# Optimization experiments

Measured on AMD Instinct MI355X. Metric: run time of the kernel, lower is better.

Reference implementation:

```python
import jax, jax.numpy as jnp
import numpy as np

N_HEADS = 16
ROPE_BASE = 10000.0


def _rope_tables(T, head_dim, dtype):
    inv_freq = 1.0 / (ROPE_BASE ** (jnp.arange(0, head_dim, 2, dtype=jnp.float32) / head_dim))
    t = jnp.arange(T, dtype=jnp.float32)
    freqs = jnp.outer(t, inv_freq)              # (T, head_dim/2)
    emb = jnp.concatenate([freqs, freqs], -1)   # (T, head_dim)
    return jnp.cos(emb).astype(dtype), jnp.sin(emb).astype(dtype)


def _rotate_half(x):
    x1, x2 = jnp.split(x, 2, axis=-1)
    return jnp.concatenate([-x2, x1], axis=-1)


def setup_inputs() -> dict:
    key = jax.random.key(0)
    k1, k2, k3 = jax.random.split(key, 3)
    B, T, C = 2, 2048, 2048
    x = jax.random.normal(k1, (B, T, C), dtype=jnp.float32)
    Wqkv = jax.random.normal(k2, (C, 3 * C), dtype=jnp.float32) * (1.0 / np.sqrt(C))
    Wproj = jax.random.normal(k3, (C, C), dtype=jnp.float32) * (1.0 / np.sqrt(C))
    return {"x": x, "Wqkv": Wqkv, "Wproj": Wproj}


def reference(x, Wqkv, Wproj):
    B, T, C = x.shape
    H = N_HEADS
    D = C // H
    qkv = jnp.einsum('btc,cd->btd', x, Wqkv)            # (B,T,3C)
    q, k, v = jnp.split(qkv, 3, axis=-1)
    # (B,T,C) -> (B,H,T,D)
    q = q.reshape(B, T, H, D).transpose(0, 2, 1, 3)
    k = k.reshape(B, T, H, D).transpose(0, 2, 1, 3)
    v = v.reshape(B, T, H, D).transpose(0, 2, 1, 3)
    cos, sin = _rope_tables(T, D, x.dtype)              # (T,D) each
    q = q * cos + _rotate_half(q) * sin
    k = k * cos + _rotate_half(k) * sin
    scale = 1.0 / jnp.sqrt(jnp.asarray(D, x.dtype))
    att = jnp.einsum('bhqd,bhkd->bhqk', q, k) * scale   # (B,H,T,T)
    causal = jnp.tril(jnp.ones((T, T), dtype=bool))
    att = jnp.where(causal, att, jnp.asarray(-jnp.inf, att.dtype))
    att = jax.nn.softmax(att, axis=-1)
    y = jnp.einsum('bhqk,bhkd->bhqd', att, v)           # (B,H,T,D)
    y = y.transpose(0, 2, 1, 3).reshape(B, T, C)
    return jnp.einsum('btc,cd->btd', y, Wproj)
```

## Files before the change

kernel.cpp:

```cpp
#include <hip/hip_runtime.h>
#include <stdint.h>

#define T_SEQ 2048
#define NH 16
#define HD 128
#define CC 2048
#define N3 6144
#define MM 4096

typedef short bf16x8 __attribute__((ext_vector_type(8)));
typedef float f32x4 __attribute__((ext_vector_type(4)));
typedef float f32x16 __attribute__((ext_vector_type(16)));
typedef unsigned int u32x4 __attribute__((ext_vector_type(4)));

__device__ __forceinline__ unsigned short f2bf(float f) {
  unsigned int u = __float_as_uint(f);
  u += 0x7FFF + ((u >> 16) & 1);
  return (unsigned short)(u >> 16);
}
__device__ __forceinline__ float bf2f(unsigned short h) {
  return __uint_as_float(((unsigned int)h) << 16);
}
__device__ __forceinline__ unsigned int cvt_pk_bf16(float lo, float hi) {
  unsigned int r;
  asm("v_cvt_pk_bf16_f32 %0, %1, %2" : "=v"(r) : "v"(lo), "v"(hi));
  return r;
}

__global__ __launch_bounds__(256) void k_prep(const float* __restrict__ Wqkv,
                                              unsigned short* __restrict__ WqkvT,
                                              const float* __restrict__ Wproj,
                                              unsigned short* __restrict__ WprojT,
                                              const float* __restrict__ x,
                                              unsigned short* __restrict__ xb) {
  __shared__ float tile[32][33];
  const int bi = blockIdx.x;
  const int tx = threadIdx.x & 31, ty = threadIdx.x >> 5;
  if (bi < 16384) {
    const float* in;
    unsigned short* out;
    int k0, n0, N;
    if (bi < 12288) {
      in = Wqkv; out = WqkvT; N = N3;
      k0 = (bi & 63) * 32; n0 = (bi >> 6) * 32;
    } else {
      in = Wproj; out = WprojT; N = CC;
      int b2 = bi - 12288;
      k0 = (b2 & 63) * 32; n0 = (b2 >> 6) * 32;
    }
    #pragma unroll
    for (int r = ty; r < 32; r += 8)
      tile[r][tx] = in[(size_t)(k0 + r) * N + n0 + tx];
    __syncthreads();
    #pragma unroll
    for (int r = ty; r < 32; r += 8)
      out[(size_t)(n0 + r) * CC + k0 + tx] = f2bf(tile[tx][r]);
  } else {
    int i = (bi - 16384) * 256 + threadIdx.x;
    float4 v = ((const float4*)x)[i];
    ushort4 o;
    o.x = f2bf(v.x); o.y = f2bf(v.y); o.z = f2bf(v.z); o.w = f2bf(v.w);
    ((ushort4*)xb)[i] = o;
  }
}

template<int NJ, int EPI, int MMAJ>
__global__ __launch_bounds__(512, 1) void k_gemm8(const unsigned short* __restrict__ A,
                                                  const unsigned short* __restrict__ Bt,
                                                  float* __restrict__ C,
                                                  unsigned short* __restrict__ qo,
                                                  unsigned short* __restrict__ ko,
                                                  unsigned short* __restrict__ vto,
                                                  int M, int N, int K) {
  constexpr int BU = NJ / 2;
  constexpr int DSTRIDE = (1 + BU) * 16384;
  extern __shared__ __align__(16) char lds[];
  const int tid = threadIdx.x;
  const int lane = tid & 63;
  const int lr = lane & 15, lg = lane >> 4;
  const int wave = tid >> 6;
  const int wm = wave >> 2, wn = wave & 3;
  const int nwg = gridDim.x;
  const int bid = blockIdx.x;
  const int wg = (bid & 7) * (nwg >> 3) + (bid >> 3);
  const int GX = M >> 7;
  const int GN = N / (NJ * 64);
  const int mt = MMAJ ? (wg % GX) : (wg / GN);
  const int nt = MMAJ ? (wg / GX) : (wg % GN);
  const int m0 = mt * 128, n0 = nt * NJ * 64;
  const int NT = K >> 6;

  auto STAGE = [&](int d, int op, int h, int t) {
    const unsigned short* src = op ? Bt : A;
    const int r0 = (op ? n0 + h * 128 : m0);
    const int kc = t * 64;
    char* base = lds + d * DSTRIDE + op * 16384 + h * 16384;
    #pragma unroll
    for (int l = 0; l < 2; ++l) {
      int p = (l * 512 + tid) * 16;
      int qq = p ^ (((p >> 7) & 7) << 4);
      const unsigned short* g = src + (size_t)(r0 + (qq >> 7)) * K + kc + ((qq & 127) >> 1);
      __builtin_amdgcn_global_load_lds(
          (const __attribute__((address_space(1))) void*)g,
          (__attribute__((address_space(3))) void*)(base + (l * 512 + (tid & 448)) * 16),
          16, 0, 0);
    }
  };
  auto RD = [&](int d, int op, int row, int kb) -> bf16x8 {
    const char* base = lds + d * DSTRIDE + op * 16384;
    int p = row * 128 + kb;
    p ^= ((p >> 7) & 7) << 4;
    return *(const bf16x8*)(base + p);
  };

  f32x4 acc[4][NJ];
  #pragma unroll
  for (int i = 0; i < 4; ++i)
    #pragma unroll
    for (int j = 0; j < NJ; ++j) acc[i][j] = (f32x4){0.f, 0.f, 0.f, 0.f};

  bf16x8 bfrg[NJ][2];

#define GPH(D, MI, READB, DOST, SD, SO, SH, ST, VM)                                      \
  {                                                                                      \
    if (READB) {                                                                         \
      _Pragma("unroll")                                                                  \
      for (int nj = 0; nj < NJ; ++nj)                                                    \
        _Pragma("unroll")                                                                \
        for (int ks = 0; ks < 2; ++ks)                                                   \
          bfrg[nj][ks] = RD(D, 1, wn * NJ * 16 + nj * 16 + lr, ks * 64 + lg * 16);       \
    }                                                                                    \
    bf16x8 af[2];                                                                        \
    _Pragma("unroll")                                                                    \
    for (int ks = 0; ks < 2; ++ks)                                                       \
      af[ks] = RD(D, 0, wm * 64 + (MI) * 16 + lr, ks * 64 + lg * 16);                    \
    if (DOST) STAGE(SD, SO, SH, ST);                                                     \
    __builtin_amdgcn_s_barrier();                                                        \
    asm volatile("s_waitcnt lgkmcnt(0)" ::: "memory");                                   \
    __builtin_amdgcn_s_setprio(1);                                                       \
    _Pragma("unroll")                                                                    \
    for (int nj = 0; nj < NJ; ++nj)                                                      \
      _Pragma("unroll")                                                                  \
      for (int ks = 0; ks < 2; ++ks)                                                     \
        acc[MI][nj] = __builtin_amdgcn_mfma_f32_16x16x32_bf16(af[ks], bfrg[nj][ks], acc[MI][nj], 0, 0, 0); \
    __builtin_amdgcn_s_setprio(0);                                                       \
    if ((VM) == 6) asm volatile("s_waitcnt vmcnt(6)" ::: "memory");                      \
    if ((VM) == 4) asm volatile("s_waitcnt vmcnt(4)" ::: "memory");                      \
    __builtin_amdgcn_s_barrier();                                                        \
  }

#define GPM(D, MIB, READB, VM, ...)                                                      \
  {                                                                                      \
    if (READB) {                                                                         \
      _Pragma("unroll")                                                                  \
      for (int nj = 0; nj < NJ; ++nj)                                                    \
        _Pragma("unroll")                                                                \
        for (int ks = 0; ks < 2; ++ks)                                                   \
          bfrg[nj][ks] = RD(D, 1, wn * NJ * 16 + nj * 16 + lr, ks * 64 + lg * 16);       \
    }                                                                                    \
    bf16x8 af2[2][2];                                                                    \
    _Pragma("unroll")                                                                    \
    for (int mm = 0; mm < 2; ++mm)                                                       \
      _Pragma("unroll")                                                                  \
      for (int ks = 0; ks < 2; ++ks)                                                     \
        af2[mm][ks] = RD(D, 0, wm * 64 + (MIB + mm) * 16 + lr, ks * 64 + lg * 16);       \
    __VA_ARGS__                                                                          \
    __builtin_amdgcn_s_barrier();                                                        \
    asm volatile("s_waitcnt lgkmcnt(0)" ::: "memory");                                   \
    __builtin_amdgcn_s_setprio(1);                                                       \
    _Pragma("unroll")                                                                    \
    for (int mm = 0; mm < 2; ++mm)                                                       \
      _Pragma("unroll")                                                                  \
      for (int nj = 0; nj < NJ; ++nj)                                                    \
        _Pragma("unroll")                                                                \
        for (int ks = 0; ks < 2; ++ks)                                                   \
          acc[MIB + mm][nj] = __builtin_amdgcn_mfma_f32_16x16x32_bf16(af2[mm][ks], bfrg[nj][ks], acc[MIB + mm][nj], 0, 0, 0); \
    __builtin_amdgcn_s_setprio(0);                                                       \
    if ((VM) == 4) asm volatile("s_waitcnt vmcnt(4)" ::: "memory");                      \
    if ((VM) == 2) asm volatile("s_waitcnt vmcnt(2)" ::: "memory");                      \
    __builtin_amdgcn_s_barrier();                                                        \
  }

  const int t1 = NT > 1 ? 1 : 0;
  #pragma unroll
  for (int h = 0; h < BU; ++h) STAGE(0, 1, h, 0);
  STAGE(0, 0, 0, 0);
  #pragma unroll
  for (int h = 0; h < BU; ++h) STAGE(1, 1, h, t1);
  if (NJ == 6) asm volatile("s_waitcnt vmcnt(6)" ::: "memory");
  else         asm volatile("s_waitcnt vmcnt(4)" ::: "memory");
  __builtin_amdgcn_s_barrier();

  for (int it = 0; it < (NT >> 1); ++it) {
    const int tb  = 2 * it + 1;
    const int ta1 = min(2 * it + 2, NT - 1);
    const int tb1 = min(2 * it + 3, NT - 1);
    if constexpr (NJ == 6) {
      GPH(0, 0, true,  true, 1, 0, 0, tb,  -1)
      GPH(0, 1, false, true, 0, 1, 0, ta1, -1)
      GPH(0, 2, false, true, 0, 1, 1, ta1, -1)
      GPH(0, 3, false, true, 0, 1, 2, ta1,  6)
      GPH(1, 0, true,  true, 0, 0, 0, ta1, -1)
      GPH(1, 1, false, true, 1, 1, 0, tb1, -1)
      GPH(1, 2, false, true, 1, 1, 1, tb1, -1)
      GPH(1, 3, false, true, 1, 1, 2, tb1,  6)
    } else {
      GPM(0, 0, true,  -1, STAGE(1, 0, 0, tb);)
      GPM(0, 2, false,  2, STAGE(0, 1, 0, ta1);)
      GPM(1, 0, true,  -1, STAGE(0, 1, 1, ta1); STAGE(0, 0, 0, ta1);)
      GPM(1, 2, false,  4, STAGE(1, 1, 0, tb1); STAGE(1, 1, 1, tb1);)
    }
  }
#undef GPH
#undef GPM

  if (EPI == 0) {
    #pragma unroll
    for (int mi = 0; mi < 4; ++mi)
      #pragma unroll
      for (int nj = 0; nj < NJ; ++nj)
        #pragma unroll
        for (int j = 0; j < 4; ++j) {
          int m = m0 + wm * 64 + mi * 16 + lg * 4 + j;
          int n = n0 + wn * NJ * 16 + nj * 16 + lr;
          C[(size_t)m * N + n] = acc[mi][nj][j];
        }
  } else {
    const bool hasV = (n0 + NJ * 64 > 4096);
    if (hasV) __builtin_amdgcn_s_barrier();
    unsigned short* ldv = (unsigned short*)lds;
    #pragma unroll
    for (int mi = 0; mi < 4; ++mi) {
      #pragma unroll
      for (int nj = 0; nj < NJ; ++nj) {
        int lcol = wn * NJ * 16 + nj * 16 + lr;
        int n = n0 + lcol;
        int which = n >> 11, cc = n & 2047;
        int h = cc >> 7, d = cc & 127;
        int lrow = wm * 64 + mi * 16 + lg * 4;
        int m_base = m0 + lrow;
        int b = m_base >> 11, t = m_base & 2047;
        if (which == 2) {
          #pragma unroll
          for (int j = 0; j < 4; ++j)
            ldv[lcol * 136 + lrow + j] = f2bf(acc[mi][nj][j]);
        } else {
          unsigned short* dst = which == 0 ? qo : ko;
          #pragma unroll
          for (int j = 0; j < 4; ++j)
            dst[(((size_t)(b * NH + h)) * T_SEQ + t + j) * HD + d] = f2bf(acc[mi][nj][j]);
        }
      }
    }
    if (hasV) {
      __builtin_amdgcn_s_barrier();
      const int bb = m0 >> 11, t0 = m0 & 2047;
      for (int pass = 0; pass < (NJ * 64) / 32; ++pass) {
        int col = pass * 32 + (tid >> 4);
        int rg = tid & 15;
        int n = n0 + col;
        if ((n >> 11) == 2) {
          int cc = n & 2047, h = cc >> 7, d = cc & 127;
          bf16x8 vv = *(const bf16x8*)(ldv + col * 136 + rg * 8);
          *(bf16x8*)(vto + (((size_t)(bb * NH + h) * HD + d) * T_SEQ + t0 + rg * 8)) = vv;
        }
      }
    }
  }
}

__global__ __launch_bounds__(256) void k_rope(unsigned short* __restrict__ q,
                                              unsigned short* __restrict__ k) {
  int i = blockIdx.x * 256 + threadIdx.x;
  int d = i & 63;
  int t = (i >> 6) & (T_SEQ - 1);
  int bh = i >> 17;
  float invf = exp2f((float)(-2 * d) * (13.287712379549449f / 128.f));
  float ang = (float)t * invf;
  float c = cosf(ang), s = sinf(ang);
  size_t base = ((size_t)bh * T_SEQ + t) * HD + d;
  const float scale = 0.12751741562076117f;
  float q1 = bf2f(q[base]), q2 = bf2f(q[base + 64]);
  q[base]      = f2bf((q1 * c - q2 * s) * scale);
  q[base + 64] = f2bf((q2 * c + q1 * s) * scale);
  float k1 = bf2f(k[base]), k2 = bf2f(k[base + 64]);
  k[base]      = f2bf(k1 * c - k2 * s);
  k[base + 64] = f2bf(k2 * c + k1 * s);
}

__global__ __launch_bounds__(512, 1) void k_attn(const unsigned short* __restrict__ Q,
                                                 const unsigned short* __restrict__ K,
                                                 const unsigned short* __restrict__ Vt,
                                                 unsigned short* __restrict__ Y) {
  extern __shared__ __align__(16) char alds[];
  char* Kls = alds;
  char* Vls = alds + 65536;
  const int id = blockIdx.x;
  const int bh = id & 31;
  const int qtl = 15 - (id >> 5);
  const int b = bh >> 4, h = bh & 15;
  const int tid = threadIdx.x, wv = tid >> 6, lane = tid & 63;
  const int l31 = lane & 31, hh = lane >> 5;
  const int par = wv >> 2;
  const int wq = wv & 3;
  const int q0 = qtl * 128;
  const int qglob = q0 + wq * 32 + l31;
  const unsigned short* Qb = Q + (size_t)bh * T_SEQ * HD;
  const unsigned short* Kb = K + (size_t)bh * T_SEQ * HD;
  const unsigned short* Vb = Vt + (size_t)bh * HD * T_SEQ;

  auto STAGEK = [&](int tk, int s) {
    char* base = Kls + s * 16384;
    #pragma unroll
    for (int ch = 0; ch < 2; ++ch) {
      int p = (ch * 512 + tid) * 16;
      int q = p ^ (((p >> 8) & 7) << 4);
      const unsigned short* g = Kb + (size_t)(tk + (q >> 8)) * HD + ((q & 255) >> 1);
      __builtin_amdgcn_global_load_lds(
          (const __attribute__((address_space(1))) void*)g,
          (__attribute__((address_space(3))) void*)(base + (ch * 512 + (tid & 448)) * 16),
          16, 0, 0);
    }
  };
  auto STAGEV = [&](int tk, int s) {
    char* base = Vls + s * 16384;
    #pragma unroll
    for (int ch = 0; ch < 2; ++ch) {
      int p = (ch * 512 + tid) * 16;
      int q = p ^ (((p >> 7) & 7) << 4);
      const unsigned short* g = Vb + (size_t)(q >> 7) * T_SEQ + tk + ((q & 127) >> 1);
      __builtin_amdgcn_global_load_lds(
          (const __attribute__((address_space(1))) void*)g,
          (__attribute__((address_space(3))) void*)(base + (ch * 512 + (tid & 448)) * 16),
          16, 0, 0);
    }
  };

  bf16x8 qfr[8];
  #pragma unroll
  for (int c = 0; c < 8; ++c)
    qfr[c] = *(const bf16x8*)(Qb + (size_t)qglob * HD + c * 16 + hh * 8);

  f32x16 oacc[4];
  #pragma unroll
  for (int dt = 0; dt < 4; ++dt)
    #pragma unroll
    for (int r = 0; r < 16; ++r) oacc[dt][r] = 0.f;
  float mrun = -1e30f, lrun = 0.f;

  STAGEK(0, 0); STAGEV(0, 0);
  STAGEK(64, 1); STAGEV(64, 1);
  asm volatile("s_waitcnt vmcnt(0)" ::: "memory");
  __syncthreads();

  for (int u = 0; u <= qtl; ++u) {
    if (u < qtl) {
      STAGEK((2 * u + 2) * 64, (2 * u + 2) & 3); STAGEV((2 * u + 2) * 64, (2 * u + 2) & 3);
      STAGEK((2 * u + 3) * 64, (2 * u + 3) & 3); STAGEV((2 * u + 3) * 64, (2 * u + 3) & 3);
    }
    const int jt = 2 * u + par;
    const int slot = jt & 3;

    f32x16 sacc[2];
    #pragma unroll
    for (int t = 0; t < 2; ++t)
      #pragma unroll
      for (int r = 0; r < 16; ++r) sacc[t][r] = 0.f;
    {
      const char* kbase = Kls + slot * 16384;
      #pragma unroll
      for (int t = 0; t < 2; ++t) {
        bf16x8 kf8[8];
        #pragma unroll
        for (int s = 0; s < 8; ++s) {
          int row = t * 32 + l31;
          int byte = (row * 256 + s * 32 + hh * 16) ^ ((row & 7) << 4);
          kf8[s] = *(const bf16x8*)(kbase + byte);
        }
        __builtin_amdgcn_s_setprio(1);
        #pragma unroll
        for (int s = 0; s < 8; ++s)
          sacc[t] = __builtin_amdgcn_mfma_f32_32x32x16_bf16(kf8[s], qfr[s], sacc[t], 0, 0, 0);
        __builtin_amdgcn_s_setprio(0);
      }
    }

    if (jt >= 2 * qtl) {
      #pragma unroll
      for (int t = 0; t < 2; ++t)
        #pragma unroll
        for (int r = 0; r < 16; ++r) {
          int kg = jt * 64 + t * 32 + (r & 3) + 8 * (r >> 2) + 4 * hh;
          if (kg > qglob) sacc[t][r] = -1e30f;
        }
    }

    float pmax = sacc[0][0];
    #pragma unroll
    for (int r = 1; r < 16; ++r) pmax = fmaxf(pmax, sacc[0][r]);
    #pragma unroll
    for (int r = 0; r < 16; ++r) pmax = fmaxf(pmax, sacc[1][r]);
    pmax = fmaxf(pmax, __shfl_xor(pmax, 32));

    if (__any(pmax > mrun + 8.0f)) {
      float mnew = fmaxf(mrun, pmax);
      float osc = exp2f(mrun - mnew);
      lrun *= osc;
      mrun = mnew;
      #pragma unroll
      for (int r = 0; r < 16; ++r) {
        int qr = (r & 3) + 8 * (r >> 2) + 4 * hh;
        float sr = __shfl(osc, qr);
        #pragma unroll
        for (int dt = 0; dt < 4; ++dt) oacc[dt][r] *= sr;
      }
    }

    unsigned int pk[16];
    float rsum = 0.f;
    #pragma unroll
    for (int t = 0; t < 2; ++t)
      #pragma unroll
      for (int i = 0; i < 8; ++i) {
        float p0 = exp2f(sacc[t][2 * i] - mrun);
        float p1 = exp2f(sacc[t][2 * i + 1] - mrun);
        rsum += p0 + p1;
        pk[t * 8 + i] = cvt_pk_bf16(p0, p1);
      }
    rsum += __shfl_xor(rsum, 32);
    lrun += rsum;

    bf16x8 pa[4];
    #pragma unroll
    for (int c = 0; c < 4; ++c) {
      int base = (c >> 1) * 8 + (c & 1) * 4;
      unsigned int s0 = hh == 0 ? pk[base + 2] : pk[base + 0];
      unsigned int s1 = hh == 0 ? pk[base + 3] : pk[base + 1];
      unsigned int r0 = __shfl_xor((int)s0, 32);
      unsigned int r1 = __shfl_xor((int)s1, 32);
      u32x4 f;
      f[0] = hh == 0 ? pk[base + 0] : r0;
      f[1] = hh == 0 ? pk[base + 1] : r1;
      f[2] = hh == 0 ? r0 : pk[base + 2];
      f[3] = hh == 0 ? r1 : pk[base + 3];
      pa[c] = *(bf16x8*)&f;
    }

    {
      const char* vbase = Vls + slot * 16384;
      __builtin_amdgcn_s_setprio(1);
      #pragma unroll
      for (int dt = 0; dt < 4; ++dt) {
        #pragma unroll
        for (int c = 0; c < 4; ++c) {
          int row = dt * 32 + l31;
          int byte = (row * 128 + c * 32 + hh * 16) ^ ((row & 7) << 4);
          bf16x8 vf = *(const bf16x8*)(vbase + byte);
          oacc[dt] = __builtin_amdgcn_mfma_f32_32x32x16_bf16(pa[c], vf, oacc[dt], 0, 0, 0);
        }
      }
      __builtin_amdgcn_s_setprio(0);
    }

    asm volatile("s_waitcnt vmcnt(0)" ::: "memory");
    __syncthreads();
  }

  float* obuf  = (float*)alds;
  float* mlbuf = (float*)(alds + 65536);
  if (par == 1) {
    mlbuf[(wq * 64 + lane) * 2 + 0] = mrun;
    mlbuf[(wq * 64 + lane) * 2 + 1] = lrun;
    float* ob = obuf + wq * 4096;
    #pragma unroll
    for (int dt = 0; dt < 4; ++dt)
      #pragma unroll
      for (int r = 0; r < 16; ++r)
        ob[(dt * 16 + r) * 64 + lane] = oacc[dt][r];
  }
  __syncthreads();
  if (par == 0) {
    float mo = mlbuf[(wq * 64 + lane) * 2 + 0];
    float lo = mlbuf[(wq * 64 + lane) * 2 + 1];
    float mm = fmaxf(mrun, mo);
    float se = exp2f(mrun - mm), so = exp2f(mo - mm);
    float lt = lrun * se + lo * so;
    float linv = 1.0f / lt;
    const float* ob = obuf + wq * 4096;
    #pragma unroll
    for (int r = 0; r < 16; ++r) {
      int qr = (r & 3) + 8 * (r >> 2) + 4 * hh;
      float se_r = __shfl(se, qr);
      float so_r = __shfl(so, qr);
      float li_r = __shfl(linv, qr);
      int qg = q0 + wq * 32 + qr;
      size_t base = ((size_t)b * T_SEQ + qg) * CC + h * HD;
      #pragma unroll
      for (int dt = 0; dt < 4; ++dt) {
        float oo = ob[(dt * 16 + r) * 64 + lane];
        Y[base + dt * 32 + l31] = f2bf((oacc[dt][r] * se_r + oo * so_r) * li_r);
      }
    }
  }
}

extern "C" void kernel_launch(void* const* d_in, const int* in_sizes, int n_in,
                              void* d_out, int out_size, void* d_ws, size_t ws_size,
                              hipStream_t stream) {
  const float* x     = (const float*)d_in[0];
  const float* Wqkv  = (const float*)d_in[1];
  const float* Wproj = (const float*)d_in[2];
  float* out = (float*)d_out;
  char* ws = (char*)d_ws;
  const size_t MB = 1024 * 1024;
  unsigned short* WqkvT  = (unsigned short*)(ws + 0);
  unsigned short* WprojT = (unsigned short*)(ws + 24 * MB);
  unsigned short* xb     = (unsigned short*)(ws + 32 * MB);
  unsigned short* y      = xb;
  unsigned short* q      = (unsigned short*)(ws + 48 * MB);
  unsigned short* k      = (unsigned short*)(ws + 64 * MB);
  unsigned short* vt     = (unsigned short*)(ws + 80 * MB);

  k_prep<<<dim3(24576), 256, 0, stream>>>(Wqkv, WqkvT, Wproj, WprojT, x, xb);
  k_gemm8<6, 1, 1><<<dim3((MM / 128) * (N3 / 384)), 512, 131072, stream>>>(
      xb, WqkvT, nullptr, q, k, vt, MM, N3, CC);
  k_rope<<<(32 * T_SEQ * 64) / 256, 256, 0, stream>>>(q, k);
  k_attn<<<dim3(512), 512, 131072, stream>>>(q, k, vt, y);
  k_gemm8<4, 0, 0><<<dim3((MM / 128) * (CC / 256)), 512, 98304, stream>>>(
      y, WprojT, out, nullptr, nullptr, nullptr, MM, CC, CC);
}
```

Measured before the change: 248.0 us.

## Fuse RoPE and Q scaling into QKV GEMM epilogue via LDS staging

Removes the standalone RoPE kernel by applying rotary embedding and the query scale inside the QKV GEMM epilogue. All outputs, not only V, are now staged through LDS so each thread can read the paired rotate-half column. A cos/sin table is precomputed in the prep kernel and stored temporarily in the output buffer. This saves a full read-modify-write pass over Q and K and one launch. The cost is a second barrier for every tile and strided scalar global stores for Q and K in the epilogue.

```diff
diff --git a/kernel.cpp b/kernel.cpp
--- a/kernel.cpp
+++ b/kernel.cpp
@@ -32,7 +32,8 @@
                                               const float* __restrict__ Wproj,
                                               unsigned short* __restrict__ WprojT,
                                               const float* __restrict__ x,
-                                              unsigned short* __restrict__ xb) {
+                                              unsigned short* __restrict__ xb,
+                                              float2* __restrict__ tbl) {
   __shared__ float tile[32][33];
   const int bi = blockIdx.x;
   const int tx = threadIdx.x & 31, ty = threadIdx.x >> 5;
@@ -55,12 +56,19 @@
     #pragma unroll
     for (int r = ty; r < 32; r += 8)
       out[(size_t)(n0 + r) * CC + k0 + tx] = f2bf(tile[tx][r]);
-  } else {
+  } else if (bi < 24576) {
     int i = (bi - 16384) * 256 + threadIdx.x;
     float4 v = ((const float4*)x)[i];
     ushort4 o;
     o.x = f2bf(v.x); o.y = f2bf(v.y); o.z = f2bf(v.z); o.w = f2bf(v.w);
     ((ushort4*)xb)[i] = o;
+  } else {
+    int idx = (bi - 24576) * 256 + threadIdx.x;
+    int dd = idx >> 11;
+    int t = idx & 2047;
+    float invf = exp2f(-(float)dd * (13.287712379549449f / 64.f));
+    float ang = (float)t * invf;
+    tbl[idx] = make_float2(cosf(ang), sinf(ang));
   }
 }
 
@@ -71,6 +79,7 @@
                                                   unsigned short* __restrict__ qo,
                                                   unsigned short* __restrict__ ko,
                                                   unsigned short* __restrict__ vto,
+                                                  const float2* __restrict__ tbl,
                                                   int M, int N, int K) {
   constexpr int BU = NJ / 2;
   constexpr int DSTRIDE = (1 + BU) * 16384;
@@ -226,66 +235,49 @@
           C[(size_t)m * N + n] = acc[mi][nj][j];
         }
   } else {
-    const bool hasV = (n0 + NJ * 64 > 4096);
-    if (hasV) __builtin_amdgcn_s_barrier();
+    __builtin_amdgcn_s_barrier();
     unsigned short* ldv = (unsigned short*)lds;
     #pragma unroll
     for (int mi = 0; mi < 4; ++mi) {
       #pragma unroll
       for (int nj = 0; nj < NJ; ++nj) {
         int lcol = wn * NJ * 16 + nj * 16 + lr;
-        int n = n0 + lcol;
-        int which = n >> 11, cc = n & 2047;
-        int h = cc >> 7, d = cc & 127;
         int lrow = wm * 64 + mi * 16 + lg * 4;
-        int m_base = m0 + lrow;
-        int b = m_base >> 11, t = m_base & 2047;
-        if (which == 2) {
-          #pragma unroll
-          for (int j = 0; j < 4; ++j)
-            ldv[lcol * 136 + lrow + j] = f2bf(acc[mi][nj][j]);
-        } else {
-          unsigned short* dst = which == 0 ? qo : ko;
-          #pragma unroll
-          for (int j = 0; j < 4; ++j)
-            dst[(((size_t)(b * NH + h)) * T_SEQ + t + j) * HD + d] = f2bf(acc[mi][nj][j]);
+        #pragma unroll
+        for (int j = 0; j < 4; ++j)
+          ldv[lcol * 136 + lrow + j] = f2bf(acc[mi][nj][j]);
+      }
+    }
+    __builtin_amdgcn_s_barrier();
+    const int bb = m0 >> 11, t0 = m0 & 2047;
+    for (int pass = 0; pass < (NJ * 64) / 32; ++pass) {
+      int col = pass * 32 + (tid >> 4);
+      int rg = tid & 15;
+      int n = n0 + col;
+      int which = n >> 11;
+      int cc = n & 2047, h = cc >> 7, d = cc & 127;
+      if (which == 2) {
+        bf16x8 vv = *(const bf16x8*)(ldv + col * 136 + rg * 8);
+        *(bf16x8*)(vto + (((size_t)(bb * NH + h) * HD + d) * T_SEQ + t0 + rg * 8)) = vv;
+      } else {
+        int dd = d & 63;
+        int colp = (d < 64) ? col + 64 : col - 64;
+        float sign = (d < 64) ? -1.f : 1.f;
+        float scl = (which == 0) ? 0.12751741562076117f : 1.0f;
+        unsigned short* dst = (which == 0) ? qo : ko;
+        bf16x8 ow = *(const bf16x8*)(ldv + col * 136 + rg * 8);
+        bf16x8 pr = *(const bf16x8*)(ldv + colp * 136 + rg * 8);
+        size_t dbase = ((size_t)(bb * NH + h) * T_SEQ + t0 + rg * 8) * HD + d;
+        #pragma unroll
+        for (int j = 0; j < 8; ++j) {
+          float2 cs = tbl[(dd << 11) + t0 + rg * 8 + j];
+          float o = bf2f((unsigned short)ow[j]);
+          float p = bf2f((unsigned short)pr[j]);
+          dst[dbase + (size_t)j * HD] = f2bf((o * cs.x + sign * p * cs.y) * scl);
         }
       }
     }
-    if (hasV) {
-      __builtin_amdgcn_s_barrier();
-      const int bb = m0 >> 11, t0 = m0 & 2047;
-      for (int pass = 0; pass < (NJ * 64) / 32; ++pass) {
-        int col = pass * 32 + (tid >> 4);
-        int rg = tid & 15;
-        int n = n0 + col;
-        if ((n >> 11) == 2) {
-          int cc = n & 2047, h = cc >> 7, d = cc & 127;
-          bf16x8 vv = *(const bf16x8*)(ldv + col * 136 + rg * 8);
-          *(bf16x8*)(vto + (((size_t)(bb * NH + h) * HD + d) * T_SEQ + t0 + rg * 8)) = vv;
-        }
-      }
-    }
-  }
-}
-
-__global__ __launch_bounds__(256) void k_rope(unsigned short* __restrict__ q,
-                                              unsigned short* __restrict__ k) {
-  int i = blockIdx.x * 256 + threadIdx.x;
-  int d = i & 63;
-  int t = (i >> 6) & (T_SEQ - 1);
-  int bh = i >> 17;
-  float invf = exp2f((float)(-2 * d) * (13.287712379549449f / 128.f));
-  float ang = (float)t * invf;
-  float c = cosf(ang), s = sinf(ang);
-  size_t base = ((size_t)bh * T_SEQ + t) * HD + d;
-  const float scale = 0.12751741562076117f;
-  float q1 = bf2f(q[base]), q2 = bf2f(q[base + 64]);
-  q[base]      = f2bf((q1 * c - q2 * s) * scale);
-  q[base + 64] = f2bf((q2 * c + q1 * s) * scale);
-  float k1 = bf2f(k[base]), k2 = bf2f(k[base + 64]);
-  k[base]      = f2bf(k1 * c - k2 * s);
-  k[base + 64] = f2bf(k2 * c + k1 * s);
+  }
 }
 
 __global__ __launch_bounds__(512, 1) void k_attn(const unsigned short* __restrict__ Q,
@@ -520,12 +512,12 @@
   unsigned short* q      = (unsigned short*)(ws + 48 * MB);
   unsigned short* k      = (unsigned short*)(ws + 64 * MB);
   unsigned short* vt     = (unsigned short*)(ws + 80 * MB);
-
-  k_prep<<<dim3(24576), 256, 0, stream>>>(Wqkv, WqkvT, Wproj, WprojT, x, xb);
+  float2* tbl = (float2*)d_out;
+
+  k_prep<<<dim3(25088), 256, 0, stream>>>(Wqkv, WqkvT, Wproj, WprojT, x, xb, tbl);
   k_gemm8<6, 1, 1><<<dim3((MM / 128) * (N3 / 384)), 512, 131072, stream>>>(
-      xb, WqkvT, nullptr, q, k, vt, MM, N3, CC);
-  k_rope<<<(32 * T_SEQ * 64) / 256, 256, 0, stream>>>(q, k);
+      xb, WqkvT, nullptr, q, k, vt, tbl, MM, N3, CC);
   k_attn<<<dim3(512), 512, 131072, stream>>>(q, k, vt, y);
   k_gemm8<4, 0, 0><<<dim3((MM / 128) * (CC / 256)), 512, 98304, stream>>>(
-      y, WprojT, out, nullptr, nullptr, nullptr, MM, CC, CC);
-}
+      y, WprojT, out, nullptr, nullptr, nullptr, nullptr, MM, CC, CC);
+}
```

New measurement: 271.9 us. +9.6%, slower.
